# Kernel optimization log

Measured on AMD Instinct MI355X. Metric: run time of the kernel, lower is better.

Reference implementation:

```python
import jax, jax.numpy as jnp
import numpy as np

HOP = 2
N_NODES = 50000
D_FEAT = 64
N_NNZ = 800000
N_QEDGES = 32768


def setup_inputs() -> dict:
    key = jax.random.key(0)
    k1, k2, k3, k4, k5 = jax.random.split(key, 5)
    x = jax.random.normal(k1, (N_NODES, D_FEAT), dtype=jnp.float32)
    # degrees must be strictly positive (reciprocal / rsqrt / sqrt applied)
    deg = 1.0 + 63.0 * jax.random.uniform(k2, (N_NODES, 1), dtype=jnp.float32)
    adj_row = jnp.sort(jax.random.randint(k3, (N_NNZ,), 0, N_NODES, dtype=jnp.int32))
    adj_col = jax.random.randint(k4, (N_NNZ,), 0, N_NODES, dtype=jnp.int32)
    edge = jax.random.randint(k5, (2, N_QEDGES), 0, N_NODES, dtype=jnp.int32)
    return {"x": x, "deg": deg, "adj_row": adj_row, "adj_col": adj_col, "edge": edge}


def reference(x, deg, adj_row, adj_col, edge):
    N, D = x.shape
    degrev = 1.0 / deg                      # [N,1]
    # fused degree feature expansion: [N, 3D]
    x3 = jnp.concatenate((x, x * jax.lax.rsqrt(deg), x * jnp.sqrt(deg)), axis=1)

    def spmm(v):  # unweighted adj_t @ v via gather + segment-sum
        return jax.ops.segment_sum(v[adj_col], adj_row, num_segments=N)

    xs = [x3, degrev * spmm(x3)]
    for _ in range(2, HOP + 1):  # Chebyshev-like recurrence
        xs.append(degrev * spmm(xs[-1]) - xs[-2])
    h = jnp.concatenate(xs, axis=1)              # [N, (hop+1)*3*D]
    h = h.reshape(N, 3 * (HOP + 1), D)           # unflatten(1, (-1, D))
    h = jnp.transpose(h, (0, 2, 1))              # [N, D, 3*(hop+1)]
    return h[edge]                               # [2, E_q, D, 3*(hop+1)]
```

## Files before the change

### kernel.cpp

```cpp
#include <hip/hip_runtime.h>

#define N_NODES 50000
#define D_FEAT 64
#define N_NNZ 800000
#define N_ENT 65536

typedef unsigned int uint32;
typedef unsigned short ushort16;

#define PLANE_U4 ((size_t)N_NODES * 8)
#define PLANE_US ((size_t)N_NODES * 64)

__device__ __forceinline__ uint32 rne1(float a) {
    uint32 u = __float_as_uint(a);
    return (u + 0x7FFFu + ((u >> 16) & 1u)) >> 16;
}
__device__ __forceinline__ uint32 rne2(float a, float b) {
    return rne1(a) | (rne1(b) << 16);
}
__device__ __forceinline__ float bf_lo(uint32 u) { return __uint_as_float(u << 16); }
__device__ __forceinline__ float bf_hi(uint32 u) { return __uint_as_float(u & 0xFFFF0000u); }
__device__ __forceinline__ void unpack8(const uint4 v, float* f) {
    f[0] = bf_lo(v.x); f[1] = bf_hi(v.x);
    f[2] = bf_lo(v.y); f[3] = bf_hi(v.y);
    f[4] = bf_lo(v.z); f[5] = bf_hi(v.z);
    f[6] = bf_lo(v.w); f[7] = bf_hi(v.w);
}
__device__ __forceinline__ float bf1(ushort16 u) { return __uint_as_float(((uint32)u) << 16); }

__global__ void build_rowptr_scal(const int* __restrict__ adj_row,
                                  const float* __restrict__ deg,
                                  int* __restrict__ row_ptr,
                                  float4* __restrict__ scal,
                                  int nnz, int n) {
    int r = blockIdx.x * blockDim.x + threadIdx.x;
    if (r > n) return;
    int lo = 0, hi = nnz;
    while (lo < hi) {
        int mid = (lo + hi) >> 1;
        if (adj_row[mid] < r) lo = mid + 1; else hi = mid;
    }
    row_ptr[r] = lo;
    if (r < n) {
        float d  = deg[r];
        float sq = sqrtf(d);
        scal[r] = make_float4(1.0f / d, 1.0f / sq, sq, 0.0f);
    }
}

__global__ __launch_bounds__(256) void pack_x(const float2* __restrict__ x2,
                                              uint32* __restrict__ xh, int npair) {
    int i = blockIdx.x * blockDim.x + threadIdx.x;
    if (i >= npair) return;
    float2 v = x2[i];
    xh[i] = rne2(v.x, v.y);
}

__global__ __launch_bounds__(256) void spmm1_kernel(
    const uint4* __restrict__ xh, const float4* __restrict__ scal,
    const int* __restrict__ adj_col, const int* __restrict__ row_ptr,
    uint4* __restrict__ y1h, int n) {
    int t    = threadIdx.x & 63;
    int f    = t & 7;
    int r    = (blockIdx.x * 4 + (threadIdx.x >> 6)) * 8 + (t >> 3);
    if (r >= n) return;

    int s = row_ptr[r], e = row_ptr[r + 1];
    int cnt = e - s;
    float a0[8], a1[8], a2[8];
#pragma unroll
    for (int j = 0; j < 8; ++j) { a0[j] = 0.f; a1[j] = 0.f; a2[j] = 0.f; }

    int i = 0;
    for (; i + 2 <= cnt; i += 2) {
        int c0 = adj_col[s + i];
        int c1 = adj_col[s + i + 1];
        uint4 xv0 = xh[(size_t)c0 * 8 + f];
        uint4 xv1 = xh[(size_t)c1 * 8 + f];
        float4 sc0 = scal[c0];
        float4 sc1 = scal[c1];
        float xf0[8], xf1[8];
        unpack8(xv0, xf0); unpack8(xv1, xf1);
#pragma unroll
        for (int j = 0; j < 8; ++j) {
            a0[j] += xf0[j];
            a1[j] += xf0[j] * sc0.y;
            a2[j] += xf0[j] * sc0.z;
            a0[j] += xf1[j];
            a1[j] += xf1[j] * sc1.y;
            a2[j] += xf1[j] * sc1.z;
        }
    }
    if (i < cnt) {
        int c = adj_col[s + i];
        uint4 xv = xh[(size_t)c * 8 + f];
        float4 sc = scal[c];
        float xf[8]; unpack8(xv, xf);
#pragma unroll
        for (int j = 0; j < 8; ++j) {
            a0[j] += xf[j];
            a1[j] += xf[j] * sc.y;
            a2[j] += xf[j] * sc.z;
        }
    }

    float dr = scal[r].x;
    size_t base = (size_t)r * 8 + f;
    y1h[base]               = make_uint4(rne2(a0[0]*dr, a0[1]*dr), rne2(a0[2]*dr, a0[3]*dr),
                                         rne2(a0[4]*dr, a0[5]*dr), rne2(a0[6]*dr, a0[7]*dr));
    y1h[base + PLANE_U4]    = make_uint4(rne2(a1[0]*dr, a1[1]*dr), rne2(a1[2]*dr, a1[3]*dr),
                                         rne2(a1[4]*dr, a1[5]*dr), rne2(a1[6]*dr, a1[7]*dr));
    y1h[base + 2*PLANE_U4]  = make_uint4(rne2(a2[0]*dr, a2[1]*dr), rne2(a2[2]*dr, a2[3]*dr),
                                         rne2(a2[4]*dr, a2[5]*dr), rne2(a2[6]*dr, a2[7]*dr));
}

__global__ __launch_bounds__(256) void spmm2_kernel(
    const float4* __restrict__ x4, const float4* __restrict__ scal,
    const int* __restrict__ adj_col, const int* __restrict__ row_ptr,
    const uint4* __restrict__ y1h, uint4* __restrict__ y2h, int n) {
    int t = threadIdx.x & 63;
    int f = t & 7;
    int r = (blockIdx.x * 4 + (threadIdx.x >> 6)) * 8 + (t >> 3);
    int g = blockIdx.y;
    if (r >= n) return;
    const uint4* yp = y1h + (size_t)g * PLANE_U4;

    int s = row_ptr[r], e = row_ptr[r + 1];
    int cnt = e - s;
    float a[8];
#pragma unroll
    for (int j = 0; j < 8; ++j) a[j] = 0.f;

    int i = 0;
    for (; i + 4 <= cnt; i += 4) {
        int c0 = adj_col[s + i];
        int c1 = adj_col[s + i + 1];
        int c2 = adj_col[s + i + 2];
        int c3 = adj_col[s + i + 3];
        uint4 b0 = yp[(size_t)c0 * 8 + f];
        uint4 b1 = yp[(size_t)c1 * 8 + f];
        uint4 b2 = yp[(size_t)c2 * 8 + f];
        uint4 b3 = yp[(size_t)c3 * 8 + f];
        float f0[8], f1[8], f2[8], f3[8];
        unpack8(b0, f0); unpack8(b1, f1); unpack8(b2, f2); unpack8(b3, f3);
#pragma unroll
        for (int j = 0; j < 8; ++j)
            a[j] += (f0[j] + f1[j]) + (f2[j] + f3[j]);
    }
    for (; i < cnt; ++i) {
        int c = adj_col[s + i];
        uint4 b = yp[(size_t)c * 8 + f];
        float fv[8]; unpack8(b, fv);
#pragma unroll
        for (int j = 0; j < 8; ++j) a[j] += fv[j];
    }

    float4 sc = scal[r];
    float w = (g == 0) ? 1.0f : ((g == 1) ? sc.y : sc.z);
    float4 xa = x4[(size_t)r * 16 + f * 2];
    float4 xb = x4[(size_t)r * 16 + f * 2 + 1];
    float xr[8] = {xa.x, xa.y, xa.z, xa.w, xb.x, xb.y, xb.z, xb.w};
    float v[8];
#pragma unroll
    for (int j = 0; j < 8; ++j) v[j] = sc.x * a[j] - xr[j] * w;

    uint4* yr = y2h + (size_t)g * PLANE_U4 + (size_t)r * 8 + f;
    yr[0] = make_uint4(rne2(v[0], v[1]), rne2(v[2], v[3]),
                       rne2(v[4], v[5]), rne2(v[6], v[7]));
}

__global__ __launch_bounds__(256) void gather_kernel(
    const float* __restrict__ x, const float4* __restrict__ scal,
    const int* __restrict__ edge, const ushort16* __restrict__ y1h,
    const ushort16* __restrict__ y2h, float* __restrict__ out) {
    __shared__ __align__(16) float lds[4][576];
    int wave = threadIdx.x >> 6;
    int t    = threadIdx.x & 63;
    int ent  = blockIdx.x * 4 + wave;

    int n = edge[ent];
    float4 sc = scal[n];
    float xv = x[n * D_FEAT + t];
    size_t nb = (size_t)n * 64 + t;

    float h[9];
    h[0] = xv;                      h[1] = xv * sc.y;                h[2] = xv * sc.z;
    h[3] = bf1(y1h[nb]);            h[4] = bf1(y1h[nb + PLANE_US]);  h[5] = bf1(y1h[nb + 2*PLANE_US]);
    h[6] = bf1(y2h[nb]);            h[7] = bf1(y2h[nb + PLANE_US]);  h[8] = bf1(y2h[nb + 2*PLANE_US]);

#pragma unroll
    for (int g = 0; g < 9; ++g) lds[wave][t * 9 + g] = h[g];
    __syncthreads();

    const float4* l4 = (const float4*)lds[wave];
    float4* o4 = (float4*)(out + (size_t)ent * 576);
    o4[t]      = l4[t];
    o4[t + 64] = l4[t + 64];
    if (t < 16) o4[t + 128] = l4[t + 128];
}

extern "C" void kernel_launch(void* const* d_in, const int* in_sizes, int n_in,
                              void* d_out, int out_size, void* d_ws, size_t ws_size,
                              hipStream_t stream) {
    const float* x       = (const float*)d_in[0];
    const float* deg     = (const float*)d_in[1];
    const int*   adj_row = (const int*)d_in[2];
    const int*   adj_col = (const int*)d_in[3];
    const int*   edge    = (const int*)d_in[4];
    float* out = (float*)d_out;

    char* ws = (char*)d_ws;
    size_t off = 0;
    int*    row_ptr = (int*)ws;            off = ((size_t)(N_NODES + 1) * 4 + 255) & ~(size_t)255;
    float4* scal    = (float4*)(ws + off); off += (size_t)N_NODES * 16;
    uint32* xh      = (uint32*)(ws + off); off += (size_t)N_NODES * 64 * 2;
    off = (off + 255) & ~(size_t)255;
    uint4*  y1h     = (uint4*)(ws + off);  off += (size_t)N_NODES * 192 * 2;
    off = (off + 255) & ~(size_t)255;
    uint4*  y2h     = (uint4*)(ws + off);

    int nblk = (N_NODES + 31) / 32;

    build_rowptr_scal<<<(N_NODES + 1 + 255) / 256, 256, 0, stream>>>(
        adj_row, deg, row_ptr, scal, N_NNZ, N_NODES);
    pack_x<<<(N_NODES * 32 + 255) / 256, 256, 0, stream>>>(
        (const float2*)x, xh, N_NODES * 32);
    spmm1_kernel<<<nblk, 256, 0, stream>>>(
        (const uint4*)xh, scal, adj_col, row_ptr, y1h, N_NODES);
    spmm2_kernel<<<dim3(nblk, 3), 256, 0, stream>>>(
        (const float4*)x, scal, adj_col, row_ptr, y1h, y2h, N_NODES);
    gather_kernel<<<N_ENT / 4, 256, 0, stream>>>(
        x, scal, edge, (const ushort16*)y1h, (const ushort16*)y2h, out);
}
```

Measured before the change: 255.0 us.

## Sort rows by degree and compute hop-2 SpMM only for queried nodes

Adds flag, histogram, prefix and scatter kernels that bucket rows by nonzero count, descending, so waves in the SpMM kernels process rows of similar length. The second SpMM is restricted to nodes that appear in the query edge list, since only those rows of the hop-2 result are gathered. This is meant to cut load imbalance and skip unneeded hop-2 rows. In exchange it adds three small kernel launches, a serial single-thread prefix, global atomics, and indirect row indexing that scatters output writes.

```diff
diff --git a/kernel.cpp b/kernel.cpp
--- a/kernel.cpp
+++ b/kernel.cpp
@@ -32,6 +32,9 @@
                                   const float* __restrict__ deg,
                                   int* __restrict__ row_ptr,
                                   float4* __restrict__ scal,
+                                  int* __restrict__ flag,
+                                  int* __restrict__ hist1,
+                                  int* __restrict__ hist2,
                                   int nnz, int n) {
     int r = blockIdx.x * blockDim.x + threadIdx.x;
     if (r > n) return;
@@ -45,25 +48,67 @@
         float d  = deg[r];
         float sq = sqrtf(d);
         scal[r] = make_float4(1.0f / d, 1.0f / sq, sq, 0.0f);
-    }
+        flag[r] = 0;
+    }
+    if (r < 64) { hist1[r] = 0; hist2[r] = 0; }
 }
 
 __global__ __launch_bounds__(256) void pack_x(const float2* __restrict__ x2,
-                                              uint32* __restrict__ xh, int npair) {
+                                              uint32* __restrict__ xh,
+                                              const int* __restrict__ edge,
+                                              int* __restrict__ flag, int npair) {
     int i = blockIdx.x * blockDim.x + threadIdx.x;
     if (i >= npair) return;
     float2 v = x2[i];
     xh[i] = rne2(v.x, v.y);
+    if (i < N_ENT) flag[edge[i]] = 1;
+}
+
+__global__ __launch_bounds__(256) void hist_kernel(
+    const int* __restrict__ row_ptr, const int* __restrict__ flag,
+    int* __restrict__ hist1, int* __restrict__ hist2, int n) {
+    int r = blockIdx.x * blockDim.x + threadIdx.x;
+    if (r >= n) return;
+    int b = min(row_ptr[r + 1] - row_ptr[r], 63);
+    atomicAdd(&hist1[b], 1);
+    if (flag[r]) atomicAdd(&hist2[b], 1);
+}
+
+__global__ void prefix_kernel(const int* __restrict__ hist1,
+                              const int* __restrict__ hist2,
+                              int* __restrict__ cur1, int* __restrict__ cur2,
+                              int* __restrict__ n_needed) {
+    if (threadIdx.x == 0) {
+        int acc = 0;
+        for (int b = 63; b >= 0; --b) { cur1[b] = acc; acc += hist1[b]; }
+        int acc2 = 0;
+        for (int b = 63; b >= 0; --b) { cur2[b] = acc2; acc2 += hist2[b]; }
+        *n_needed = acc2;
+    }
+}
+
+__global__ __launch_bounds__(256) void scatter_kernel(
+    const int* __restrict__ row_ptr, const int* __restrict__ flag,
+    int* __restrict__ cur1, int* __restrict__ cur2,
+    int* __restrict__ perm1, int* __restrict__ perm2, int n) {
+    int r = blockIdx.x * blockDim.x + threadIdx.x;
+    if (r >= n) return;
+    int b = min(row_ptr[r + 1] - row_ptr[r], 63);
+    int p = atomicAdd(&cur1[b], 1);
+    perm1[p] = r;
+    if (flag[r]) { int q = atomicAdd(&cur2[b], 1); perm2[q] = r; }
 }
 
 __global__ __launch_bounds__(256) void spmm1_kernel(
     const uint4* __restrict__ xh, const float4* __restrict__ scal,
     const int* __restrict__ adj_col, const int* __restrict__ row_ptr,
+    const int* __restrict__ perm1,
     uint4* __restrict__ y1h, int n) {
     int t    = threadIdx.x & 63;
     int f    = t & 7;
-    int r    = (blockIdx.x * 4 + (threadIdx.x >> 6)) * 8 + (t >> 3);
-    if (r >= n) return;
+    int idx  = (blockIdx.x * 4 + (threadIdx.x >> 6)) * 8 + (t >> 3);
+    if (idx >= n) return;
+    int r = perm1[idx];
 
     int s = row_ptr[r], e = row_ptr[r + 1];
     int cnt = e - s;
@@ -117,12 +162,14 @@
 __global__ __launch_bounds__(256) void spmm2_kernel(
     const float4* __restrict__ x4, const float4* __restrict__ scal,
     const int* __restrict__ adj_col, const int* __restrict__ row_ptr,
-    const uint4* __restrict__ y1h, uint4* __restrict__ y2h, int n) {
+    const int* __restrict__ perm2, const int* __restrict__ n_needed,
+    const uint4* __restrict__ y1h, uint4* __restrict__ y2h) {
     int t = threadIdx.x & 63;
     int f = t & 7;
-    int r = (blockIdx.x * 4 + (threadIdx.x >> 6)) * 8 + (t >> 3);
+    int idx = (blockIdx.x * 4 + (threadIdx.x >> 6)) * 8 + (t >> 3);
     int g = blockIdx.y;
-    if (r >= n) return;
+    if (idx >= *n_needed) return;
+    int r = perm2[idx];
     const uint4* yp = y1h + (size_t)g * PLANE_U4;
 
     int s = row_ptr[r], e = row_ptr[r + 1];
@@ -217,18 +264,33 @@
     off = (off + 255) & ~(size_t)255;
     uint4*  y1h     = (uint4*)(ws + off);  off += (size_t)N_NODES * 192 * 2;
     off = (off + 255) & ~(size_t)255;
-    uint4*  y2h     = (uint4*)(ws + off);
-
+    uint4*  y2h     = (uint4*)(ws + off);  off += (size_t)N_NODES * 192 * 2;
+    off = (off + 255) & ~(size_t)255;
+    int*    flag    = (int*)(ws + off);    off += (size_t)N_NODES * 4;
+    int*    perm1   = (int*)(ws + off);    off += (size_t)N_NODES * 4;
+    int*    perm2   = (int*)(ws + off);    off += (size_t)N_NODES * 4;
+    off = (off + 255) & ~(size_t)255;
+    int*    hist1   = (int*)(ws + off);    off += 64 * 4;
+    int*    hist2   = (int*)(ws + off);    off += 64 * 4;
+    int*    cur1    = (int*)(ws + off);    off += 64 * 4;
+    int*    cur2    = (int*)(ws + off);    off += 64 * 4;
+    int*    n_need  = (int*)(ws + off);    off += 4;
+
+    int nrb = (N_NODES + 255) / 256;
     int nblk = (N_NODES + 31) / 32;
 
     build_rowptr_scal<<<(N_NODES + 1 + 255) / 256, 256, 0, stream>>>(
-        adj_row, deg, row_ptr, scal, N_NNZ, N_NODES);
+        adj_row, deg, row_ptr, scal, flag, hist1, hist2, N_NNZ, N_NODES);
     pack_x<<<(N_NODES * 32 + 255) / 256, 256, 0, stream>>>(
-        (const float2*)x, xh, N_NODES * 32);
+        (const float2*)x, xh, edge, flag, N_NODES * 32);
+    hist_kernel<<<nrb, 256, 0, stream>>>(row_ptr, flag, hist1, hist2, N_NODES);
+    prefix_kernel<<<1, 64, 0, stream>>>(hist1, hist2, cur1, cur2, n_need);
+    scatter_kernel<<<nrb, 256, 0, stream>>>(row_ptr, flag, cur1, cur2,
+                                            perm1, perm2, N_NODES);
     spmm1_kernel<<<nblk, 256, 0, stream>>>(
-        (const uint4*)xh, scal, adj_col, row_ptr, y1h, N_NODES);
+        (const uint4*)xh, scal, adj_col, row_ptr, perm1, y1h, N_NODES);
     spmm2_kernel<<<dim3(nblk, 3), 256, 0, stream>>>(
-        (const float4*)x, scal, adj_col, row_ptr, y1h, y2h, N_NODES);
+        (const float4*)x, scal, adj_col, row_ptr, perm2, n_need, y1h, y2h);
     gather_kernel<<<N_ENT / 4, 256, 0, stream>>>(
         x, scal, edge, (const ushort16*)y1h, (const ushort16*)y2h, out);
 }
```

New measurement: 596.0 us. 134% more time.

## Fuse all stages into one cooperative persistent kernel with grid syncs

Applied to the files above, without the earlier changes.

Replaces the five separate kernel launches (row pointer build, x packing, two SpMM passes, output gather) with a single cooperative kernel. Each stage becomes a grid-stride loop, and stages are separated by grid.sync(). The aim is to remove per-launch overhead and the idle gaps between kernels. In exchange the grid is capped at occupancy × 256 blocks, so fewer waves are in flight to hide gather latency. Grid-wide barriers also have their own cost, and the gather loop now needs an extra block sync on every iteration.

```diff
diff --git a/kernel.cpp b/kernel.cpp
--- a/kernel.cpp
+++ b/kernel.cpp
@@ -1,4 +1,7 @@
 #include <hip/hip_runtime.h>
+#include <hip/hip_cooperative_groups.h>
+
+namespace cg = cooperative_groups;
 
 #define N_NODES 50000
 #define D_FEAT 64
@@ -28,175 +31,187 @@
 }
 __device__ __forceinline__ float bf1(ushort16 u) { return __uint_as_float(((uint32)u) << 16); }
 
-__global__ void build_rowptr_scal(const int* __restrict__ adj_row,
-                                  const float* __restrict__ deg,
-                                  int* __restrict__ row_ptr,
-                                  float4* __restrict__ scal,
-                                  int nnz, int n) {
-    int r = blockIdx.x * blockDim.x + threadIdx.x;
-    if (r > n) return;
-    int lo = 0, hi = nnz;
-    while (lo < hi) {
-        int mid = (lo + hi) >> 1;
-        if (adj_row[mid] < r) lo = mid + 1; else hi = mid;
-    }
-    row_ptr[r] = lo;
-    if (r < n) {
-        float d  = deg[r];
-        float sq = sqrtf(d);
-        scal[r] = make_float4(1.0f / d, 1.0f / sq, sq, 0.0f);
-    }
-}
-
-__global__ __launch_bounds__(256) void pack_x(const float2* __restrict__ x2,
-                                              uint32* __restrict__ xh, int npair) {
-    int i = blockIdx.x * blockDim.x + threadIdx.x;
-    if (i >= npair) return;
-    float2 v = x2[i];
-    xh[i] = rne2(v.x, v.y);
-}
-
-__global__ __launch_bounds__(256) void spmm1_kernel(
-    const uint4* __restrict__ xh, const float4* __restrict__ scal,
-    const int* __restrict__ adj_col, const int* __restrict__ row_ptr,
-    uint4* __restrict__ y1h, int n) {
-    int t    = threadIdx.x & 63;
-    int f    = t & 7;
-    int r    = (blockIdx.x * 4 + (threadIdx.x >> 6)) * 8 + (t >> 3);
-    if (r >= n) return;
-
-    int s = row_ptr[r], e = row_ptr[r + 1];
-    int cnt = e - s;
-    float a0[8], a1[8], a2[8];
-#pragma unroll
-    for (int j = 0; j < 8; ++j) { a0[j] = 0.f; a1[j] = 0.f; a2[j] = 0.f; }
-
-    int i = 0;
-    for (; i + 2 <= cnt; i += 2) {
-        int c0 = adj_col[s + i];
-        int c1 = adj_col[s + i + 1];
-        uint4 xv0 = xh[(size_t)c0 * 8 + f];
-        uint4 xv1 = xh[(size_t)c1 * 8 + f];
-        float4 sc0 = scal[c0];
-        float4 sc1 = scal[c1];
-        float xf0[8], xf1[8];
-        unpack8(xv0, xf0); unpack8(xv1, xf1);
-#pragma unroll
-        for (int j = 0; j < 8; ++j) {
-            a0[j] += xf0[j];
-            a1[j] += xf0[j] * sc0.y;
-            a2[j] += xf0[j] * sc0.z;
-            a0[j] += xf1[j];
-            a1[j] += xf1[j] * sc1.y;
-            a2[j] += xf1[j] * sc1.z;
-        }
-    }
-    if (i < cnt) {
-        int c = adj_col[s + i];
-        uint4 xv = xh[(size_t)c * 8 + f];
-        float4 sc = scal[c];
-        float xf[8]; unpack8(xv, xf);
-#pragma unroll
-        for (int j = 0; j < 8; ++j) {
-            a0[j] += xf[j];
-            a1[j] += xf[j] * sc.y;
-            a2[j] += xf[j] * sc.z;
-        }
-    }
-
-    float dr = scal[r].x;
-    size_t base = (size_t)r * 8 + f;
-    y1h[base]               = make_uint4(rne2(a0[0]*dr, a0[1]*dr), rne2(a0[2]*dr, a0[3]*dr),
-                                         rne2(a0[4]*dr, a0[5]*dr), rne2(a0[6]*dr, a0[7]*dr));
-    y1h[base + PLANE_U4]    = make_uint4(rne2(a1[0]*dr, a1[1]*dr), rne2(a1[2]*dr, a1[3]*dr),
-                                         rne2(a1[4]*dr, a1[5]*dr), rne2(a1[6]*dr, a1[7]*dr));
-    y1h[base + 2*PLANE_U4]  = make_uint4(rne2(a2[0]*dr, a2[1]*dr), rne2(a2[2]*dr, a2[3]*dr),
-                                         rne2(a2[4]*dr, a2[5]*dr), rne2(a2[6]*dr, a2[7]*dr));
-}
-
-__global__ __launch_bounds__(256) void spmm2_kernel(
-    const float4* __restrict__ x4, const float4* __restrict__ scal,
-    const int* __restrict__ adj_col, const int* __restrict__ row_ptr,
-    const uint4* __restrict__ y1h, uint4* __restrict__ y2h, int n) {
-    int t = threadIdx.x & 63;
-    int f = t & 7;
-    int r = (blockIdx.x * 4 + (threadIdx.x >> 6)) * 8 + (t >> 3);
-    int g = blockIdx.y;
-    if (r >= n) return;
-    const uint4* yp = y1h + (size_t)g * PLANE_U4;
-
-    int s = row_ptr[r], e = row_ptr[r + 1];
-    int cnt = e - s;
-    float a[8];
-#pragma unroll
-    for (int j = 0; j < 8; ++j) a[j] = 0.f;
-
-    int i = 0;
-    for (; i + 4 <= cnt; i += 4) {
-        int c0 = adj_col[s + i];
-        int c1 = adj_col[s + i + 1];
-        int c2 = adj_col[s + i + 2];
-        int c3 = adj_col[s + i + 3];
-        uint4 b0 = yp[(size_t)c0 * 8 + f];
-        uint4 b1 = yp[(size_t)c1 * 8 + f];
-        uint4 b2 = yp[(size_t)c2 * 8 + f];
-        uint4 b3 = yp[(size_t)c3 * 8 + f];
-        float f0[8], f1[8], f2[8], f3[8];
-        unpack8(b0, f0); unpack8(b1, f1); unpack8(b2, f2); unpack8(b3, f3);
-#pragma unroll
-        for (int j = 0; j < 8; ++j)
-            a[j] += (f0[j] + f1[j]) + (f2[j] + f3[j]);
-    }
-    for (; i < cnt; ++i) {
-        int c = adj_col[s + i];
-        uint4 b = yp[(size_t)c * 8 + f];
-        float fv[8]; unpack8(b, fv);
-#pragma unroll
-        for (int j = 0; j < 8; ++j) a[j] += fv[j];
-    }
-
-    float4 sc = scal[r];
-    float w = (g == 0) ? 1.0f : ((g == 1) ? sc.y : sc.z);
-    float4 xa = x4[(size_t)r * 16 + f * 2];
-    float4 xb = x4[(size_t)r * 16 + f * 2 + 1];
-    float xr[8] = {xa.x, xa.y, xa.z, xa.w, xb.x, xb.y, xb.z, xb.w};
-    float v[8];
-#pragma unroll
-    for (int j = 0; j < 8; ++j) v[j] = sc.x * a[j] - xr[j] * w;
-
-    uint4* yr = y2h + (size_t)g * PLANE_U4 + (size_t)r * 8 + f;
-    yr[0] = make_uint4(rne2(v[0], v[1]), rne2(v[2], v[3]),
-                       rne2(v[4], v[5]), rne2(v[6], v[7]));
-}
-
-__global__ __launch_bounds__(256) void gather_kernel(
-    const float* __restrict__ x, const float4* __restrict__ scal,
-    const int* __restrict__ edge, const ushort16* __restrict__ y1h,
-    const ushort16* __restrict__ y2h, float* __restrict__ out) {
+__global__ __launch_bounds__(256, 4) void fused_all(
+    const float* __restrict__ x, const float* __restrict__ deg,
+    const int* __restrict__ adj_row, const int* __restrict__ adj_col,
+    const int* __restrict__ edge,
+    int* __restrict__ row_ptr, float4* __restrict__ scal,
+    uint32* __restrict__ xh, uint4* __restrict__ y1h, uint4* __restrict__ y2h,
+    float* __restrict__ out)
+{
     __shared__ __align__(16) float lds[4][576];
-    int wave = threadIdx.x >> 6;
-    int t    = threadIdx.x & 63;
-    int ent  = blockIdx.x * 4 + wave;
-
-    int n = edge[ent];
-    float4 sc = scal[n];
-    float xv = x[n * D_FEAT + t];
-    size_t nb = (size_t)n * 64 + t;
-
-    float h[9];
-    h[0] = xv;                      h[1] = xv * sc.y;                h[2] = xv * sc.z;
-    h[3] = bf1(y1h[nb]);            h[4] = bf1(y1h[nb + PLANE_US]);  h[5] = bf1(y1h[nb + 2*PLANE_US]);
-    h[6] = bf1(y2h[nb]);            h[7] = bf1(y2h[nb + PLANE_US]);  h[8] = bf1(y2h[nb + 2*PLANE_US]);
-
-#pragma unroll
-    for (int g = 0; g < 9; ++g) lds[wave][t * 9 + g] = h[g];
-    __syncthreads();
-
-    const float4* l4 = (const float4*)lds[wave];
-    float4* o4 = (float4*)(out + (size_t)ent * 576);
-    o4[t]      = l4[t];
-    o4[t + 64] = l4[t + 64];
-    if (t < 16) o4[t + 128] = l4[t + 128];
+    cg::grid_group grid = cg::this_grid();
+
+    const int tid      = threadIdx.x;
+    const int nthreads = gridDim.x * 256;
+    const int gthread  = blockIdx.x * 256 + tid;
+
+    for (int r = gthread; r <= N_NODES; r += nthreads) {
+        int lo = 0, hi = N_NNZ;
+        while (lo < hi) {
+            int mid = (lo + hi) >> 1;
+            if (adj_row[mid] < r) lo = mid + 1; else hi = mid;
+        }
+        row_ptr[r] = lo;
+        if (r < N_NODES) {
+            float d  = deg[r];
+            float sq = sqrtf(d);
+            scal[r] = make_float4(1.0f / d, 1.0f / sq, sq, 0.0f);
+        }
+    }
+    {
+        const float2* x2 = (const float2*)x;
+        for (int i = gthread; i < N_NODES * 32; i += nthreads) {
+            float2 v = x2[i];
+            xh[i] = rne2(v.x, v.y);
+        }
+    }
+    grid.sync();
+
+    {
+        const uint4* xh4 = (const uint4*)xh;
+        const int f        = tid & 7;
+        const int waveslot = blockIdx.x * 4 + (tid >> 6);
+        const int octet    = (tid & 63) >> 3;
+        const int rows_per = gridDim.x * 4 * 8;
+        for (int base = 0; base < N_NODES; base += rows_per) {
+            int r = base + waveslot * 8 + octet;
+            if (r < N_NODES) {
+                int s = row_ptr[r], e = row_ptr[r + 1];
+                int cnt = e - s;
+                float a0[8], a1[8], a2[8];
+#pragma unroll
+                for (int j = 0; j < 8; ++j) { a0[j] = 0.f; a1[j] = 0.f; a2[j] = 0.f; }
+                int i = 0;
+                for (; i + 2 <= cnt; i += 2) {
+                    int c0 = adj_col[s + i];
+                    int c1 = adj_col[s + i + 1];
+                    uint4 xv0 = xh4[(size_t)c0 * 8 + f];
+                    uint4 xv1 = xh4[(size_t)c1 * 8 + f];
+                    float4 sc0 = scal[c0];
+                    float4 sc1 = scal[c1];
+                    float xf0[8], xf1[8];
+                    unpack8(xv0, xf0); unpack8(xv1, xf1);
+#pragma unroll
+                    for (int j = 0; j < 8; ++j) {
+                        a0[j] += xf0[j];
+                        a1[j] += xf0[j] * sc0.y;
+                        a2[j] += xf0[j] * sc0.z;
+                        a0[j] += xf1[j];
+                        a1[j] += xf1[j] * sc1.y;
+                        a2[j] += xf1[j] * sc1.z;
+                    }
+                }
+                if (i < cnt) {
+                    int c = adj_col[s + i];
+                    uint4 xv = xh4[(size_t)c * 8 + f];
+                    float4 sc = scal[c];
+                    float xf[8]; unpack8(xv, xf);
+#pragma unroll
+                    for (int j = 0; j < 8; ++j) {
+                        a0[j] += xf[j];
+                        a1[j] += xf[j] * sc.y;
+                        a2[j] += xf[j] * sc.z;
+                    }
+                }
+                float dr = scal[r].x;
+                size_t bo = (size_t)r * 8 + f;
+                y1h[bo]              = make_uint4(rne2(a0[0]*dr, a0[1]*dr), rne2(a0[2]*dr, a0[3]*dr),
+                                                  rne2(a0[4]*dr, a0[5]*dr), rne2(a0[6]*dr, a0[7]*dr));
+                y1h[bo + PLANE_U4]   = make_uint4(rne2(a1[0]*dr, a1[1]*dr), rne2(a1[2]*dr, a1[3]*dr),
+                                                  rne2(a1[4]*dr, a1[5]*dr), rne2(a1[6]*dr, a1[7]*dr));
+                y1h[bo + 2*PLANE_U4] = make_uint4(rne2(a2[0]*dr, a2[1]*dr), rne2(a2[2]*dr, a2[3]*dr),
+                                                  rne2(a2[4]*dr, a2[5]*dr), rne2(a2[6]*dr, a2[7]*dr));
+            }
+        }
+    }
+    grid.sync();
+
+    {
+        const float4* x4 = (const float4*)x;
+        const int f        = tid & 7;
+        const int waveslot = blockIdx.x * 4 + (tid >> 6);
+        const int octet    = (tid & 63) >> 3;
+        const int rows_per = gridDim.x * 4 * 8;
+        for (int g = 0; g < 3; ++g) {
+            const uint4* yp = y1h + (size_t)g * PLANE_U4;
+            for (int base = 0; base < N_NODES; base += rows_per) {
+                int r = base + waveslot * 8 + octet;
+                if (r < N_NODES) {
+                    int s = row_ptr[r], e = row_ptr[r + 1];
+                    int cnt = e - s;
+                    float a[8];
+#pragma unroll
+                    for (int j = 0; j < 8; ++j) a[j] = 0.f;
+                    int i = 0;
+                    for (; i + 4 <= cnt; i += 4) {
+                        int c0 = adj_col[s + i];
+                        int c1 = adj_col[s + i + 1];
+                        int c2 = adj_col[s + i + 2];
+                        int c3 = adj_col[s + i + 3];
+                        uint4 b0 = yp[(size_t)c0 * 8 + f];
+                        uint4 b1 = yp[(size_t)c1 * 8 + f];
+                        uint4 b2 = yp[(size_t)c2 * 8 + f];
+                        uint4 b3 = yp[(size_t)c3 * 8 + f];
+                        float f0[8], f1[8], f2[8], f3[8];
+                        unpack8(b0, f0); unpack8(b1, f1); unpack8(b2, f2); unpack8(b3, f3);
+#pragma unroll
+                        for (int j = 0; j < 8; ++j)
+                            a[j] += (f0[j] + f1[j]) + (f2[j] + f3[j]);
+                    }
+                    for (; i < cnt; ++i) {
+                        int c = adj_col[s + i];
+                        uint4 b = yp[(size_t)c * 8 + f];
+                        float fv[8]; unpack8(b, fv);
+#pragma unroll
+                        for (int j = 0; j < 8; ++j) a[j] += fv[j];
+                    }
+                    float4 sc = scal[r];
+                    float w = (g == 0) ? 1.0f : ((g == 1) ? sc.y : sc.z);
+                    float4 xa = x4[(size_t)r * 16 + f * 2];
+                    float4 xb = x4[(size_t)r * 16 + f * 2 + 1];
+                    float xr[8] = {xa.x, xa.y, xa.z, xa.w, xb.x, xb.y, xb.z, xb.w};
+                    float v[8];
+#pragma unroll
+                    for (int j = 0; j < 8; ++j) v[j] = sc.x * a[j] - xr[j] * w;
+                    uint4* yr = y2h + (size_t)g * PLANE_U4 + (size_t)r * 8 + f;
+                    yr[0] = make_uint4(rne2(v[0], v[1]), rne2(v[2], v[3]),
+                                       rne2(v[4], v[5]), rne2(v[6], v[7]));
+                }
+            }
+        }
+    }
+    grid.sync();
+
+    {
+        const ushort16* y1s = (const ushort16*)y1h;
+        const ushort16* y2s = (const ushort16*)y2h;
+        const int wave = tid >> 6;
+        const int t    = tid & 63;
+        for (int ent0 = blockIdx.x * 4; ent0 < N_ENT; ent0 += gridDim.x * 4) {
+            int ent = ent0 + wave;
+            int n = edge[ent];
+            float4 sc = scal[n];
+            float xv = x[n * D_FEAT + t];
+            size_t nb = (size_t)n * 64 + t;
+
+            float h[9];
+            h[0] = xv;               h[1] = xv * sc.y;               h[2] = xv * sc.z;
+            h[3] = bf1(y1s[nb]);     h[4] = bf1(y1s[nb + PLANE_US]); h[5] = bf1(y1s[nb + 2*PLANE_US]);
+            h[6] = bf1(y2s[nb]);     h[7] = bf1(y2s[nb + PLANE_US]); h[8] = bf1(y2s[nb + 2*PLANE_US]);
+
+#pragma unroll
+            for (int g = 0; g < 9; ++g) lds[wave][t * 9 + g] = h[g];
+            __syncthreads();
+
+            const float4* l4 = (const float4*)lds[wave];
+            float4* o4 = (float4*)(out + (size_t)ent * 576);
+            o4[t]      = l4[t];
+            o4[t + 64] = l4[t + 64];
+            if (t < 16) o4[t + 128] = l4[t + 128];
+            __syncthreads();
+        }
+    }
 }
 
 extern "C" void kernel_launch(void* const* d_in, const int* in_sizes, int n_in,
@@ -219,16 +234,20 @@
     off = (off + 255) & ~(size_t)255;
     uint4*  y2h     = (uint4*)(ws + off);
 
-    int nblk = (N_NODES + 31) / 32;
-
-    build_rowptr_scal<<<(N_NODES + 1 + 255) / 256, 256, 0, stream>>>(
-        adj_row, deg, row_ptr, scal, N_NNZ, N_NODES);
-    pack_x<<<(N_NODES * 32 + 255) / 256, 256, 0, stream>>>(
-        (const float2*)x, xh, N_NODES * 32);
-    spmm1_kernel<<<nblk, 256, 0, stream>>>(
-        (const uint4*)xh, scal, adj_col, row_ptr, y1h, N_NODES);
-    spmm2_kernel<<<dim3(nblk, 3), 256, 0, stream>>>(
-        (const float4*)x, scal, adj_col, row_ptr, y1h, y2h, N_NODES);
-    gather_kernel<<<N_ENT / 4, 256, 0, stream>>>(
-        x, scal, edge, (const ushort16*)y1h, (const ushort16*)y2h, out);
-}
+    static int coop_grid = -1;
+    if (coop_grid < 0) {
+        int occ = 0;
+        hipOccupancyMaxActiveBlocksPerMultiprocessor(&occ, fused_all, 256, 0);
+        if (occ < 1) occ = 1;
+        if (occ > 4) occ = 4;
+        coop_grid = occ * 256;
+    }
+
+    void* kargs[] = {
+        (void*)&x, (void*)&deg, (void*)&adj_row, (void*)&adj_col, (void*)&edge,
+        (void*)&row_ptr, (void*)&scal, (void*)&xh, (void*)&y1h, (void*)&y2h,
+        (void*)&out
+    };
+    hipLaunchCooperativeKernel((void*)fused_all, dim3(coop_grid), dim3(256),
+                               kargs, 0, stream);
+}
```

Result: slower. 547.9 us (+114.8%).
